# Kernel tuning notes

Measured on AMD Instinct MI355X. Metric: run time of the kernel, lower is better.

The kernel has to match this reference:

```python
import jax, jax.numpy as jnp
import numpy as np

N_WORD, N_TOPIC, N_DOC = 50000, 2000, 50000
D_WORD, D_TOPIC, D_OUT = 256, 128, 128
E_WW, E_WT, E_WD, E_TD, E_TT = 500000, 400000, 500000, 400000, 300000


def setup_inputs() -> dict:
    key = jax.random.key(0)
    ks = jax.random.split(key, 32)
    i = iter(range(32))

    def randn(shape, scale=1.0):
        return jax.random.normal(ks[next(i)], shape, dtype=jnp.float32) * scale

    def edges(n_e, n_src, n_dst):
        src = jax.random.randint(ks[next(i)], (n_e,), 0, n_src, dtype=jnp.int32)
        dst = jax.random.randint(ks[next(i)], (n_e,), 0, n_dst, dtype=jnp.int32)
        w = jax.random.uniform(ks[next(i)], (n_e,), dtype=jnp.float32)
        return src, dst, w

    feat_word = randn((N_WORD, D_WORD))
    feat_topic = randn((N_TOPIC, D_TOPIC))
    ww_src, ww_dst, ww_w = edges(E_WW, N_WORD, N_WORD)
    wt_src, wt_dst, wt_w = edges(E_WT, N_WORD, N_TOPIC)
    wd_src, wd_dst, wd_w = edges(E_WD, N_WORD, N_DOC)
    td_src, td_dst, td_w = edges(E_TD, N_TOPIC, N_DOC)
    tt_src, tt_dst, tt_w = edges(E_TT, N_TOPIC, N_TOPIC)
    return dict(
        feat_word=feat_word, feat_topic=feat_topic,
        ww_src=ww_src, ww_dst=ww_dst, ww_w=ww_w,
        wt_src=wt_src, wt_dst=wt_dst, wt_w=wt_w,
        wd_src=wd_src, wd_dst=wd_dst, wd_w=wd_w,
        td_src=td_src, td_dst=td_dst, td_w=td_w,
        tt_src=tt_src, tt_dst=tt_dst, tt_w=tt_w,
        W_ww=randn((D_WORD, D_OUT), 0.02), b_ww=randn((D_OUT,), 0.02),
        W_wt=randn((D_WORD, D_OUT), 0.02), b_wt=randn((D_OUT,), 0.02),
        W_wd=randn((D_WORD, D_OUT), 0.02), b_wd=randn((D_OUT,), 0.02),
        W_td=randn((D_TOPIC, D_OUT), 0.02), b_td=randn((D_OUT,), 0.02),
        W_tt=randn((D_TOPIC, D_OUT), 0.02), b_tt=randn((D_OUT,), 0.02),
    )


def _mean_agg(Wh, src, dst, w, n_dst):
    # u_mul_e: gather src feature, scale by edge weight; fn.mean: divide by in-degree
    m = Wh[src] * w[:, None]                                   # [E, D_OUT]
    s = jax.ops.segment_sum(m, dst, num_segments=n_dst)        # [n_dst, D_OUT]
    deg = jax.ops.segment_sum(jnp.ones_like(w), dst, num_segments=n_dst)
    return jnp.where(deg[:, None] > 0, s / jnp.maximum(deg, 1.0)[:, None], 0.0)


def reference(feat_word, feat_topic,
              ww_src, ww_dst, ww_w, wt_src, wt_dst, wt_w,
              wd_src, wd_dst, wd_w, td_src, td_dst, td_w,
              tt_src, tt_dst, tt_w,
              W_ww, b_ww, W_wt, b_wt, W_wd, b_wd, W_td, b_td, W_tt, b_tt):
    # Per-relation projections (note: in the torch source the causal/noise
    # branches are overwritten by the plain Linear, so this is the effective math).
    Wh_ww = feat_word @ W_ww + b_ww
    Wh_wt = feat_word @ W_wt + b_wt
    Wh_wd = feat_word @ W_wd + b_wd
    Wh_td = feat_topic @ W_td + b_td
    Wh_tt = feat_topic @ W_tt + b_tt
    # mean per edge type, then cross-etype 'sum' per destination node type
    h_word = _mean_agg(Wh_ww, ww_src, ww_dst, ww_w, N_WORD)
    h_topic = (_mean_agg(Wh_wt, wt_src, wt_dst, wt_w, N_TOPIC)
               + _mean_agg(Wh_tt, tt_src, tt_dst, tt_w, N_TOPIC))
    h_doc = (_mean_agg(Wh_wd, wd_src, wd_dst, wd_w, N_DOC)
             + _mean_agg(Wh_td, td_src, td_dst, td_w, N_DOC))
    return h_word, h_topic, h_doc
```

## Files before the change

kernel.cpp:

```cpp
#include <hip/hip_runtime.h>

typedef short short8 __attribute__((ext_vector_type(8)));
typedef float floatx4 __attribute__((ext_vector_type(4)));

__device__ __forceinline__ float b2f(unsigned int u16) {
    union { unsigned int i; float f; } v;
    v.i = u16 << 16;
    return v.f;
}
__device__ __forceinline__ unsigned short f2b(float f) {
    unsigned int i = __float_as_uint(f);
    unsigned int r = (i + 0x7FFFu + ((i >> 16) & 1u)) >> 16;
    return (unsigned short)r;
}

#define N_WORD  50000
#define N_TOPIC 2000
#define N_DOC   50000
#define E_MAX   500000
#define CHAIN_END 0xFFFFFFFFu

__global__ void detect_kernel(const unsigned int* __restrict__ feat_u32,
                              unsigned int* __restrict__ flag)
{
    int cnt = 0;
    for (int i = 0; i < 256; ++i) {
        unsigned int u = feat_u32[i];
        int e = (u >> 7) & 0xFF;
        if (e >= 110 && e <= 140) ++cnt;
    }
    *flag = (cnt > 128) ? 1u : 0u;
}

__global__ __launch_bounds__(256) void swizzle_kernel(
    const void* __restrict__ W0, const void* __restrict__ W1,
    const void* __restrict__ W2, const void* __restrict__ W3,
    const void* __restrict__ W4,
    const void* __restrict__ b0, const void* __restrict__ b1,
    const void* __restrict__ b2, const void* __restrict__ b3,
    const void* __restrict__ b4,
    short8* __restrict__ D0, short8* __restrict__ D1,
    short8* __restrict__ D2, short8* __restrict__ D3,
    short8* __restrict__ D4,
    unsigned short* __restrict__ bias_out,
    const unsigned int* __restrict__ flag_p)
{
    const int w = blockIdx.y;
    const void* W; const void* bs; short8* D; int S;
    switch (w) {
        case 0: W = W0; bs = b0; D = D0; S = 8; break;
        case 1: W = W1; bs = b1; D = D1; S = 8; break;
        case 2: W = W2; bs = b2; D = D2; S = 8; break;
        case 3: W = W3; bs = b3; D = D3; S = 4; break;
        default: W = W4; bs = b4; D = D4; S = 4; break;
    }
    const int n_entries = S * 8 * 64;
    const int mode = (int)*flag_p;
    for (int e = blockIdx.x * 256 + threadIdx.x; e < n_entries; e += 8 * 256) {
        const int lane = e & 63, t = (e >> 6) & 7, s = e >> 9;
        const int q = lane >> 4, n = t * 16 + (lane & 15);
        short8 val;
#pragma unroll
        for (int j = 0; j < 8; ++j) {
            const int k = s * 32 + q * 8 + j;
            unsigned short hv = mode ? ((const unsigned short*)W)[k * 128 + n]
                                     : f2b(((const float*)W)[k * 128 + n]);
            val[j] = (short)hv;
        }
        D[e] = val;
    }
    if (blockIdx.x == 0 && threadIdx.x < 128) {
        bias_out[w * 128 + threadIdx.x] =
            mode ? ((const unsigned short*)bs)[threadIdx.x]
                 : f2b(((const float*)bs)[threadIdx.x]);
    }
}

template <int S, int NP>
__device__ __forceinline__ void gemm_body_lds(
    short8* __restrict__ Blds,
    const void* feat_, int n_rows, int bx,
    const short8* Ba, const short8* Bb, const short8* Bc,
    const unsigned short* bias_all, int ba, int bb, int bc,
    unsigned short* Oa, unsigned short* Ob, unsigned short* Oc,
    int mode_bf16)
{
    const int tid = threadIdx.x;
    const int lane = tid & 63;
    const int wave = tid >> 6;
    const int row0 = (bx * 4 + wave) * 16;
    const int m = lane & 15, q = lane >> 4;
    const int K = S * 32;
    int arow_idx = row0 + m;
    if (arow_idx >= n_rows) arow_idx = n_rows - 1;

    short8 a[S];
    if (mode_bf16) {
        const short8* arow = (const short8*)((const unsigned short*)feat_ + (size_t)arow_idx * K);
#pragma unroll
        for (int s = 0; s < S; ++s) a[s] = arow[s * 4 + q];
    } else {
        const float* arow = (const float*)feat_ + (size_t)arow_idx * K;
#pragma unroll
        for (int s = 0; s < S; ++s) {
            const float4 f0 = ((const float4*)arow)[s * 8 + q * 2];
            const float4 f1 = ((const float4*)arow)[s * 8 + q * 2 + 1];
            short8 t;
            t[0] = (short)f2b(f0.x); t[1] = (short)f2b(f0.y);
            t[2] = (short)f2b(f0.z); t[3] = (short)f2b(f0.w);
            t[4] = (short)f2b(f1.x); t[5] = (short)f2b(f1.y);
            t[6] = (short)f2b(f1.z); t[7] = (short)f2b(f1.w);
            a[s] = t;
        }
    }

    const int n_ent = S * 8 * 64;
#pragma unroll
    for (int p = 0; p < NP; ++p) {
        const short8* B = (p == 0) ? Ba : ((p == 1) ? Bb : Bc);
        const unsigned short* bias = bias_all + ((p == 0) ? ba : ((p == 1) ? bb : bc)) * 128;
        unsigned short* O = (p == 0) ? Oa : ((p == 1) ? Ob : Oc);

        for (int i = tid; i < n_ent; i += 256) Blds[i] = B[i];
        __syncthreads();

        floatx4 acc[8];
#pragma unroll
        for (int t = 0; t < 8; ++t) { acc[t][0] = 0.f; acc[t][1] = 0.f; acc[t][2] = 0.f; acc[t][3] = 0.f; }

#pragma unroll
        for (int s = 0; s < S; ++s) {
#pragma unroll
            for (int t = 0; t < 8; ++t) {
                short8 b = Blds[(s * 8 + t) * 64 + lane];
                acc[t] = __builtin_amdgcn_mfma_f32_16x16x32_bf16(a[s], b, acc[t], 0, 0, 0);
            }
        }
        __syncthreads();

#pragma unroll
        for (int t = 0; t < 8; ++t) {
            const float bb_ = b2f((unsigned int)bias[t * 16 + m]);
#pragma unroll
            for (int r = 0; r < 4; ++r) {
                const int row = row0 + q * 4 + r;
                if (row < n_rows)
                    O[(size_t)row * 128 + t * 16 + m] = f2b(acc[t][r] + bb_);
            }
        }
    }
}

__global__ __launch_bounds__(256) void gemm_all_kernel(
    const void* __restrict__ feat_word, const void* __restrict__ feat_topic,
    const short8* __restrict__ Bww, const short8* __restrict__ Bwt,
    const short8* __restrict__ Bwd, const short8* __restrict__ Btt,
    const short8* __restrict__ Btd,
    const unsigned short* __restrict__ bias_all,
    unsigned short* __restrict__ Wh_ww, unsigned short* __restrict__ Wh_wt,
    unsigned short* __restrict__ Wh_wd, unsigned short* __restrict__ Wh_tt,
    unsigned short* __restrict__ Wh_td,
    const unsigned int* __restrict__ flag_p)
{
    __shared__ short8 Blds[4096];
    const int mode = (int)*flag_p;
    if (blockIdx.x < 782) {
        gemm_body_lds<8, 3>(Blds, feat_word, N_WORD, blockIdx.x, Bww, Bwt, Bwd,
                            bias_all, 0, 1, 2, Wh_ww, Wh_wt, Wh_wd, mode);
    } else {
        gemm_body_lds<4, 2>(Blds, feat_topic, N_TOPIC, blockIdx.x - 782, Btt, Btd,
                            (const short8*)nullptr, bias_all, 4, 3, 0,
                            Wh_tt, Wh_td, (unsigned short*)nullptr, mode);
    }
}

__global__ void link5_kernel(
    const int* s0, const int* d0, const void* w0, int n0, unsigned int* h0, unsigned long long* e0,
    const int* s1, const int* d1, const void* w1, int n1, unsigned int* h1, unsigned long long* e1,
    const int* s2, const int* d2, const void* w2, int n2, unsigned int* h2, unsigned long long* e2,
    const int* s3, const int* d3, const void* w3, int n3, unsigned int* h3, unsigned long long* e3,
    const int* s4, const int* d4, const void* w4, int n4, unsigned int* h4, unsigned long long* e4,
    const unsigned int* __restrict__ flag_p)
{
    const int* src; const int* dst; const void* w_; int n;
    unsigned int* head; unsigned long long* ent; int H;
    switch (blockIdx.y) {
        case 0: src = s0; dst = d0; w_ = w0; n = n0; head = h0; ent = e0; H = 1; break;
        case 1: src = s1; dst = d1; w_ = w1; n = n1; head = h1; ent = e1; H = 4; break;
        case 2: src = s2; dst = d2; w_ = w2; n = n2; head = h2; ent = e2; H = 4; break;
        case 3: src = s3; dst = d3; w_ = w3; n = n3; head = h3; ent = e3; H = 1; break;
        default: src = s4; dst = d4; w_ = w4; n = n4; head = h4; ent = e4; H = 1; break;
    }
    int i = blockIdx.x * 256 + threadIdx.x;
    if (i >= n) return;
    const int d = dst[i];
    const unsigned int slot = (unsigned int)d * H + ((unsigned int)i & (H - 1));
    const unsigned int old = atomicExch(&head[slot], (unsigned int)i);
    const unsigned short w16 = (*flag_p) ? ((const unsigned short*)w_)[i]
                                         : f2b(((const float*)w_)[i]);
    ent[i] = ((unsigned long long)old << 32)
           | ((unsigned long long)w16 << 16)
           | (unsigned long long)(unsigned int)src[i];
}

__device__ __forceinline__ void chain8(
    const unsigned long long* __restrict__ ent,
    const unsigned short* __restrict__ Wh,
    unsigned int e, int sl, float a[8], float& cnt)
{
    while (e != CHAIN_END) {
        const unsigned long long v = ent[e];
        const unsigned int lo = (unsigned int)v;
        e = (unsigned int)(v >> 32);
        const float w = b2f(lo >> 16);
        const uint4 u = ((const uint4*)(Wh + (size_t)(lo & 0xffffu) * 128))[sl];
        a[0] += b2f(u.x & 0xffffu) * w; a[1] += b2f(u.x >> 16) * w;
        a[2] += b2f(u.y & 0xffffu) * w; a[3] += b2f(u.y >> 16) * w;
        a[4] += b2f(u.z & 0xffffu) * w; a[5] += b2f(u.z >> 16) * w;
        a[6] += b2f(u.w & 0xffffu) * w; a[7] += b2f(u.w >> 16) * w;
        cnt += 1.0f;
    }
}

__device__ __forceinline__ void write8(
    void* out, size_t off_elems, int node, int sl, const float r[8], int mode)
{
    if (mode) {
        uint4 o;
        o.x = (unsigned int)f2b(r[0]) | ((unsigned int)f2b(r[1]) << 16);
        o.y = (unsigned int)f2b(r[2]) | ((unsigned int)f2b(r[3]) << 16);
        o.z = (unsigned int)f2b(r[4]) | ((unsigned int)f2b(r[5]) << 16);
        o.w = (unsigned int)f2b(r[6]) | ((unsigned int)f2b(r[7]) << 16);
        *(uint4*)((unsigned short*)out + off_elems + (size_t)node * 128 + sl * 8) = o;
    } else {
        float* p = (float*)out + off_elems + (size_t)node * 128 + sl * 8;
        ((float4*)p)[0] = make_float4(r[0], r[1], r[2], r[3]);
        ((float4*)p)[1] = make_float4(r[4], r[5], r[6], r[7]);
    }
}

__global__ __launch_bounds__(256) void gather_dt_kernel(
    const unsigned int* __restrict__ h_wt, const unsigned long long* __restrict__ e_wt,
    const unsigned short* __restrict__ Wh_wt,
    const unsigned int* __restrict__ h_tt, const unsigned long long* __restrict__ e_tt,
    const unsigned short* __restrict__ Wh_tt,
    const unsigned int* __restrict__ h_wd, const unsigned long long* __restrict__ e_wd,
    const unsigned short* __restrict__ Wh_wd,
    const unsigned int* __restrict__ h_td, const unsigned long long* __restrict__ e_td,
    const unsigned short* __restrict__ Wh_td,
    void* __restrict__ out,
    const unsigned int* __restrict__ flag_p)
{
    const int mode = (int)*flag_p;
    const int sl = threadIdx.x & 15;

    if (blockIdx.x < 500) {
        const int wave = threadIdx.x >> 6;
        const int grp  = (threadIdx.x >> 4) & 3;
        const int node = blockIdx.x * 4 + wave;
        float r[8] = {0, 0, 0, 0, 0, 0, 0, 0};
        {
            float a[8] = {0, 0, 0, 0, 0, 0, 0, 0}; float cnt = 0.f;
            chain8(e_wt, Wh_wt, h_wt[node * 4 + grp], sl, a, cnt);
#pragma unroll
            for (int j = 0; j < 8; ++j) { a[j] += __shfl_xor(a[j], 16); a[j] += __shfl_xor(a[j], 32); }
            cnt += __shfl_xor(cnt, 16); cnt += __shfl_xor(cnt, 32);
            const float inv = (cnt > 0.f) ? 1.f / cnt : 0.f;
#pragma unroll
            for (int j = 0; j < 8; ++j) r[j] += a[j] * inv;
        }
        {
            float a[8] = {0, 0, 0, 0, 0, 0, 0, 0}; float cnt = 0.f;
            chain8(e_tt, Wh_tt, h_tt[node * 4 + grp], sl, a, cnt);
#pragma unroll
            for (int j = 0; j < 8; ++j) { a[j] += __shfl_xor(a[j], 16); a[j] += __shfl_xor(a[j], 32); }
            cnt += __shfl_xor(cnt, 16); cnt += __shfl_xor(cnt, 32);
            const float inv = (cnt > 0.f) ? 1.f / cnt : 0.f;
#pragma unroll
            for (int j = 0; j < 8; ++j) r[j] += a[j] * inv;
        }
        if (grp == 0) write8(out, (size_t)6400000, node, sl, r, mode);
    } else {
        const int sub = threadIdx.x >> 4;
        const int node = (blockIdx.x - 500) * 16 + sub;
        float r[8] = {0, 0, 0, 0, 0, 0, 0, 0};
        {
            float a[8] = {0, 0, 0, 0, 0, 0, 0, 0}; float cnt = 0.f;
            chain8(e_wd, Wh_wd, h_wd[node], sl, a, cnt);
            const float inv = (cnt > 0.f) ? 1.f / cnt : 0.f;
#pragma unroll
            for (int j = 0; j < 8; ++j) r[j] += a[j] * inv;
        }
        {
            float a[8] = {0, 0, 0, 0, 0, 0, 0, 0}; float cnt = 0.f;
            chain8(e_td, Wh_td, h_td[node], sl, a, cnt);
            const float inv = (cnt > 0.f) ? 1.f / cnt : 0.f;
#pragma unroll
            for (int j = 0; j < 8; ++j) r[j] += a[j] * inv;
        }
        write8(out, (size_t)6656000, node, sl, r, mode);
    }
}

__global__ __launch_bounds__(256) void gather_w_kernel(
    const unsigned int* __restrict__ h_ww, const unsigned long long* __restrict__ e_ww,
    const unsigned short* __restrict__ Wh_ww,
    void* __restrict__ out,
    const unsigned int* __restrict__ flag_p)
{
    const int mode = (int)*flag_p;
    const int sl = threadIdx.x & 15;
    const int sub = threadIdx.x >> 4;
    const int node = blockIdx.x * 16 + sub;
    float a[8] = {0, 0, 0, 0, 0, 0, 0, 0}; float cnt = 0.f;
    chain8(e_ww, Wh_ww, h_ww[node], sl, a, cnt);
    const float inv = (cnt > 0.f) ? 1.f / cnt : 0.f;
#pragma unroll
    for (int j = 0; j < 8; ++j) a[j] *= inv;
    write8(out, 0, node, sl, a, mode);
}

extern "C" void kernel_launch(void* const* d_in, const int* in_sizes, int n_in,
                              void* d_out, int out_size, void* d_ws, size_t ws_size,
                              hipStream_t stream)
{
    const void* feat_word  = d_in[0];
    const void* feat_topic = d_in[1];
    const int* ww_src = (const int*)d_in[2];
    const int* ww_dst = (const int*)d_in[3];
    const void* ww_w = d_in[4];
    const int* wt_src = (const int*)d_in[5];
    const int* wt_dst = (const int*)d_in[6];
    const void* wt_w = d_in[7];
    const int* wd_src = (const int*)d_in[8];
    const int* wd_dst = (const int*)d_in[9];
    const void* wd_w = d_in[10];
    const int* td_src = (const int*)d_in[11];
    const int* td_dst = (const int*)d_in[12];
    const void* td_w = d_in[13];
    const int* tt_src = (const int*)d_in[14];
    const int* tt_dst = (const int*)d_in[15];
    const void* tt_w = d_in[16];
    const void* W_ww = d_in[17];
    const void* b_ww = d_in[18];
    const void* W_wt = d_in[19];
    const void* b_wt = d_in[20];
    const void* W_wd = d_in[21];
    const void* b_wd = d_in[22];
    const void* W_td = d_in[23];
    const void* b_td = d_in[24];
    const void* W_tt = d_in[25];
    const void* b_tt = d_in[26];

    const int E_ww = in_sizes[2];
    const int E_wt = in_sizes[5];
    const int E_wd = in_sizes[8];
    const int E_td = in_sizes[11];
    const int E_tt = in_sizes[14];

    char* ws = (char*)d_ws;
    unsigned int* flag = (unsigned int*)ws;
    unsigned int* head_base = (unsigned int*)(ws + 4);
    unsigned int* h_ww = head_base;
    unsigned int* h_wt = h_ww + 50000;
    unsigned int* h_tt = h_wt + 8000;
    unsigned int* h_wd = h_tt + 8000;
    unsigned int* h_td = h_wd + 50000;
    size_t off = 4 + (size_t)166000 * 4;
    off = (off + 15) & ~(size_t)15;
    short8* Bsw_ww = (short8*)(ws + off); off += 65536;
    short8* Bsw_wt = (short8*)(ws + off); off += 65536;
    short8* Bsw_wd = (short8*)(ws + off); off += 65536;
    short8* Bsw_td = (short8*)(ws + off); off += 32768;
    short8* Bsw_tt = (short8*)(ws + off); off += 32768;
    unsigned short* bias_all = (unsigned short*)(ws + off); off += 5 * 128 * 2;
    off = (off + 15) & ~(size_t)15;
    unsigned short* Wh_ww = (unsigned short*)(ws + off); off += (size_t)N_WORD * 128 * 2;
    unsigned short* Wh_wt = (unsigned short*)(ws + off); off += (size_t)N_WORD * 128 * 2;
    unsigned short* Wh_tt = (unsigned short*)(ws + off); off += (size_t)N_TOPIC * 128 * 2;
    unsigned short* Wh_td = (unsigned short*)(ws + off); off += (size_t)N_TOPIC * 128 * 2;
    off = (off + 7) & ~(size_t)7;
    unsigned long long* e_ww = (unsigned long long*)(ws + off); off += (size_t)E_MAX * 8;
    unsigned long long* e_wt = (unsigned long long*)(ws + off); off += (size_t)E_MAX * 8;
    unsigned long long* e_tt = (unsigned long long*)(ws + off); off += (size_t)E_MAX * 8;
    unsigned long long* e_wd = (unsigned long long*)(ws + off); off += (size_t)E_MAX * 8;
    unsigned long long* e_td = (unsigned long long*)(ws + off); off += (size_t)E_MAX * 8;

    unsigned short* Wh_wd = (unsigned short*)d_out;

    detect_kernel<<<1, 1, 0, stream>>>((const unsigned int*)feat_word, flag);
    hipMemsetAsync(head_base, 0xFF, (size_t)166000 * 4, stream);

    swizzle_kernel<<<dim3(8, 5), 256, 0, stream>>>(
        W_ww, W_wt, W_wd, W_td, W_tt, b_ww, b_wt, b_wd, b_td, b_tt,
        Bsw_ww, Bsw_wt, Bsw_wd, Bsw_td, Bsw_tt, bias_all, flag);

    link5_kernel<<<dim3((E_MAX + 255) / 256, 5), 256, 0, stream>>>(
        ww_src, ww_dst, ww_w, E_ww, h_ww, e_ww,
        wt_src, wt_dst, wt_w, E_wt, h_wt, e_wt,
        tt_src, tt_dst, tt_w, E_tt, h_tt, e_tt,
        wd_src, wd_dst, wd_w, E_wd, h_wd, e_wd,
        td_src, td_dst, td_w, E_td, h_td, e_td, flag);

    gemm_all_kernel<<<782 + 32, 256, 0, stream>>>(
        feat_word, feat_topic, Bsw_ww, Bsw_wt, Bsw_wd, Bsw_tt, Bsw_td,
        bias_all, Wh_ww, Wh_wt, Wh_wd, Wh_tt, Wh_td, flag);

    gather_dt_kernel<<<500 + 3125, 256, 0, stream>>>(
        h_wt, e_wt, Wh_wt, h_tt, e_tt, Wh_tt,
        h_wd, e_wd, Wh_wd, h_td, e_td, Wh_td, d_out, flag);

    gather_w_kernel<<<3125, 256, 0, stream>>>(
        h_ww, e_ww, Wh_ww, d_out, flag);
}
```

Before: 431.7 us.

## Fuse edge-linking and projection GEMM into one launch with halved LDS tiles

Merges the linked-list construction kernel and the projection GEMM kernel into a single launch, with the edge-linking blocks appended after the GEMM blocks via a flattened 1D grid. The two phases are independent, so the memory-bound atomic linking can overlap with the MFMA GEMM and one launch boundary is removed. To keep the fused kernel's LDS footprint small (32KB instead of 64KB, which helps occupancy for the link blocks), the GEMM now streams the weight tile in two halves with extra barriers. The cost is extra __syncthreads and B reloads per projection for the word GEMM.

Result: faster. 402.4 us (-6.8%).

```diff
diff --git a/kernel.cpp b/kernel.cpp
--- a/kernel.cpp
+++ b/kernel.cpp
@@ -19,6 +19,7 @@
 #define N_DOC   50000
 #define E_MAX   500000
 #define CHAIN_END 0xFFFFFFFFu
+#define NB_GEMM 814
 
 __global__ void detect_kernel(const unsigned int* __restrict__ feat_u32,
                               unsigned int* __restrict__ flag)
@@ -114,29 +115,33 @@
         }
     }
 
-    const int n_ent = S * 8 * 64;
+    constexpr int NH = (S * 8 * 64 > 2048) ? 2 : 1;
+    constexpr int SH = S / NH;
+
 #pragma unroll
     for (int p = 0; p < NP; ++p) {
         const short8* B = (p == 0) ? Ba : ((p == 1) ? Bb : Bc);
         const unsigned short* bias = bias_all + ((p == 0) ? ba : ((p == 1) ? bb : bc)) * 128;
         unsigned short* O = (p == 0) ? Oa : ((p == 1) ? Ob : Oc);
 
-        for (int i = tid; i < n_ent; i += 256) Blds[i] = B[i];
-        __syncthreads();
-
         floatx4 acc[8];
 #pragma unroll
         for (int t = 0; t < 8; ++t) { acc[t][0] = 0.f; acc[t][1] = 0.f; acc[t][2] = 0.f; acc[t][3] = 0.f; }
 
 #pragma unroll
-        for (int s = 0; s < S; ++s) {
-#pragma unroll
-            for (int t = 0; t < 8; ++t) {
-                short8 b = Blds[(s * 8 + t) * 64 + lane];
-                acc[t] = __builtin_amdgcn_mfma_f32_16x16x32_bf16(a[s], b, acc[t], 0, 0, 0);
+        for (int h = 0; h < NH; ++h) {
+            __syncthreads();
+            for (int i = tid; i < SH * 8 * 64; i += 256) Blds[i] = B[h * (SH * 8 * 64) + i];
+            __syncthreads();
+#pragma unroll
+            for (int s = 0; s < SH; ++s) {
+#pragma unroll
+                for (int t = 0; t < 8; ++t) {
+                    short8 b = Blds[(s * 8 + t) * 64 + lane];
+                    acc[t] = __builtin_amdgcn_mfma_f32_16x16x32_bf16(a[h * SH + s], b, acc[t], 0, 0, 0);
+                }
             }
         }
-        __syncthreads();
 
 #pragma unroll
         for (int t = 0; t < 8; ++t) {
@@ -151,7 +156,7 @@
     }
 }
 
-__global__ __launch_bounds__(256) void gemm_all_kernel(
+__global__ __launch_bounds__(256) void link_gemm_kernel(
     const void* __restrict__ feat_word, const void* __restrict__ feat_topic,
     const short8* __restrict__ Bww, const short8* __restrict__ Bwt,
     const short8* __restrict__ Bwd, const short8* __restrict__ Btt,
@@ -160,21 +165,6 @@
     unsigned short* __restrict__ Wh_ww, unsigned short* __restrict__ Wh_wt,
     unsigned short* __restrict__ Wh_wd, unsigned short* __restrict__ Wh_tt,
     unsigned short* __restrict__ Wh_td,
-    const unsigned int* __restrict__ flag_p)
-{
-    __shared__ short8 Blds[4096];
-    const int mode = (int)*flag_p;
-    if (blockIdx.x < 782) {
-        gemm_body_lds<8, 3>(Blds, feat_word, N_WORD, blockIdx.x, Bww, Bwt, Bwd,
-                            bias_all, 0, 1, 2, Wh_ww, Wh_wt, Wh_wd, mode);
-    } else {
-        gemm_body_lds<4, 2>(Blds, feat_topic, N_TOPIC, blockIdx.x - 782, Btt, Btd,
-                            (const short8*)nullptr, bias_all, 4, 3, 0,
-                            Wh_tt, Wh_td, (unsigned short*)nullptr, mode);
-    }
-}
-
-__global__ void link5_kernel(
     const int* s0, const int* d0, const void* w0, int n0, unsigned int* h0, unsigned long long* e0,
     const int* s1, const int* d1, const void* w1, int n1, unsigned int* h1, unsigned long long* e1,
     const int* s2, const int* d2, const void* w2, int n2, unsigned int* h2, unsigned long long* e2,
@@ -182,22 +172,39 @@
     const int* s4, const int* d4, const void* w4, int n4, unsigned int* h4, unsigned long long* e4,
     const unsigned int* __restrict__ flag_p)
 {
+    __shared__ short8 Blds[2048];
+    const int mode = (int)*flag_p;
+
+    if (blockIdx.x < NB_GEMM) {
+        if (blockIdx.x < 782) {
+            gemm_body_lds<8, 3>(Blds, feat_word, N_WORD, blockIdx.x, Bww, Bwt, Bwd,
+                                bias_all, 0, 1, 2, Wh_ww, Wh_wt, Wh_wd, mode);
+        } else {
+            gemm_body_lds<4, 2>(Blds, feat_topic, N_TOPIC, blockIdx.x - 782, Btt, Btd,
+                                (const short8*)nullptr, bias_all, 4, 3, 0,
+                                Wh_tt, Wh_td, (unsigned short*)nullptr, mode);
+        }
+        return;
+    }
+
+    int lb = blockIdx.x - NB_GEMM;
+    const int nb0 = (n0 + 255) >> 8, nb1 = (n1 + 255) >> 8, nb2 = (n2 + 255) >> 8,
+              nb3 = (n3 + 255) >> 8;
     const int* src; const int* dst; const void* w_; int n;
     unsigned int* head; unsigned long long* ent; int H;
-    switch (blockIdx.y) {
-        case 0: src = s0; dst = d0; w_ = w0; n = n0; head = h0; ent = e0; H = 1; break;
-        case 1: src = s1; dst = d1; w_ = w1; n = n1; head = h1; ent = e1; H = 4; break;
-        case 2: src = s2; dst = d2; w_ = w2; n = n2; head = h2; ent = e2; H = 4; break;
-        case 3: src = s3; dst = d3; w_ = w3; n = n3; head = h3; ent = e3; H = 1; break;
-        default: src = s4; dst = d4; w_ = w4; n = n4; head = h4; ent = e4; H = 1; break;
-    }
-    int i = blockIdx.x * 256 + threadIdx.x;
+    if (lb < nb0)      { src = s0; dst = d0; w_ = w0; n = n0; head = h0; ent = e0; H = 1; }
+    else if ((lb -= nb0) < nb1) { src = s1; dst = d1; w_ = w1; n = n1; head = h1; ent = e1; H = 4; }
+    else if ((lb -= nb1) < nb2) { src = s2; dst = d2; w_ = w2; n = n2; head = h2; ent = e2; H = 4; }
+    else if ((lb -= nb2) < nb3) { src = s3; dst = d3; w_ = w3; n = n3; head = h3; ent = e3; H = 1; }
+    else { lb -= nb3;  src = s4; dst = d4; w_ = w4; n = n4; head = h4; ent = e4; H = 1; }
+
+    const int i = lb * 256 + threadIdx.x;
     if (i >= n) return;
     const int d = dst[i];
     const unsigned int slot = (unsigned int)d * H + ((unsigned int)i & (H - 1));
     const unsigned int old = atomicExch(&head[slot], (unsigned int)i);
-    const unsigned short w16 = (*flag_p) ? ((const unsigned short*)w_)[i]
-                                         : f2b(((const float*)w_)[i]);
+    const unsigned short w16 = mode ? ((const unsigned short*)w_)[i]
+                                    : f2b(((const float*)w_)[i]);
     ent[i] = ((unsigned long long)old << 32)
            | ((unsigned long long)w16 << 16)
            | (unsigned long long)(unsigned int)src[i];
@@ -395,17 +402,18 @@
         W_ww, W_wt, W_wd, W_td, W_tt, b_ww, b_wt, b_wd, b_td, b_tt,
         Bsw_ww, Bsw_wt, Bsw_wd, Bsw_td, Bsw_tt, bias_all, flag);
 
-    link5_kernel<<<dim3((E_MAX + 255) / 256, 5), 256, 0, stream>>>(
+    const int nb_link = ((E_ww + 255) / 256) + ((E_wt + 255) / 256) +
+                        ((E_tt + 255) / 256) + ((E_wd + 255) / 256) +
+                        ((E_td + 255) / 256);
+    link_gemm_kernel<<<NB_GEMM + nb_link, 256, 0, stream>>>(
+        feat_word, feat_topic, Bsw_ww, Bsw_wt, Bsw_wd, Bsw_tt, Bsw_td,
+        bias_all, Wh_ww, Wh_wt, Wh_wd, Wh_tt, Wh_td,
         ww_src, ww_dst, ww_w, E_ww, h_ww, e_ww,
         wt_src, wt_dst, wt_w, E_wt, h_wt, e_wt,
         tt_src, tt_dst, tt_w, E_tt, h_tt, e_tt,
         wd_src, wd_dst, wd_w, E_wd, h_wd, e_wd,
         td_src, td_dst, td_w, E_td, h_td, e_td, flag);
 
-    gemm_all_kernel<<<782 + 32, 256, 0, stream>>>(
-        feat_word, feat_topic, Bsw_ww, Bsw_wt, Bsw_wd, Bsw_tt, Bsw_td,
-        bias_all, Wh_ww, Wh_wt, Wh_wd, Wh_tt, Wh_td, flag);
-
     gather_dt_kernel<<<500 + 3125, 256, 0, stream>>>(
         h_wt, e_wt, Wh_wt, h_tt, e_tt, Wh_tt,
         h_wd, e_wd, Wh_wd, h_td, e_td, Wh_td, d_out, flag);
```
